# Optimization experiments

Hardware: AMD Instinct MI355X
Metric: run time of the kernel (lower is better)

## Reference

```python
import jax, jax.numpy as jnp
import numpy as np

INPUT_DIM = 1024; HID = 512; DSTATE = 64; EXPAND = 2; HDIM = 32; NHEAD = 8; DFF = 1024
DIN = EXPAND * HID          # 1024 inner dim
NH = DIN // HDIM            # 32 heads
G = 1; DCONV = 4            # ngroups, depthwise conv kernel
CONV_DIM = DIN + 2 * G * DSTATE          # 1152 (x, B, C go through conv)
DPROJ = 2 * DIN + 2 * G * DSTATE + NH    # 2208 (z, xBC, dt)
B = 2; L = 4096


def rmsnorm(x, w, eps=1e-5):
    return x * jax.lax.rsqrt(jnp.mean(x * x, axis=-1, keepdims=True) + eps) * w


def layernorm(x, w, b, eps=1e-5):
    m = jnp.mean(x, axis=-1, keepdims=True)
    v = jnp.mean((x - m) ** 2, axis=-1, keepdims=True)
    return (x - m) * jax.lax.rsqrt(v + eps) * w + b


def mamba_block(x, Wi, cw, cb, dtb, Alog, Dp, nw, Wo):
    # Mamba-2 style selective scan block (SISO, ngroups=1)
    Bb, Ln, _ = x.shape
    zxbcdt = x @ Wi                                   # [B,L,DPROJ]
    z = zxbcdt[..., :DIN]
    xBC = zxbcdt[..., DIN:DIN + CONV_DIM]
    dt = zxbcdt[..., DIN + CONV_DIM:]                 # [B,L,NH]
    # causal depthwise conv1d + silu
    xBC = jnp.transpose(xBC, (0, 2, 1))               # [B,C,L]
    xBC = jax.lax.conv_general_dilated(xBC, cw, (1,), [(DCONV - 1, 0)],
                                       feature_group_count=CONV_DIM) + cb[None, :, None]
    xBC = jax.nn.silu(jnp.transpose(xBC, (0, 2, 1)))
    xs = xBC[..., :DIN].reshape(Bb, Ln, NH, HDIM)     # [B,L,H,P]
    Bm = xBC[..., DIN:DIN + DSTATE]                   # [B,L,N]
    Cm = xBC[..., DIN + DSTATE:]                      # [B,L,N]
    dt = jax.nn.softplus(dt + dtb)                    # [B,L,H]
    decay = jnp.exp(dt * (-jnp.exp(Alog)))            # [B,L,H]
    dtx = dt[..., None] * xs                          # [B,L,H,P]

    def step(h, inp):
        dec, dx, Bt, Ct = inp                         # [B,H],[B,H,P],[B,N],[B,N]
        h = h * dec[:, :, None, None] + dx[..., None] * Bt[:, None, None, :]
        return h, jnp.einsum('bhpn,bn->bhp', h, Ct)

    h0 = jnp.zeros((Bb, NH, HDIM, DSTATE), x.dtype)
    _, ys = jax.lax.scan(step, h0, (jnp.moveaxis(decay, 1, 0), jnp.moveaxis(dtx, 1, 0),
                                    jnp.moveaxis(Bm, 1, 0), jnp.moveaxis(Cm, 1, 0)))
    y = jnp.moveaxis(ys, 0, 1) + Dp[None, None, :, None] * xs
    y = y.reshape(Bb, Ln, DIN)
    return rmsnorm(y * jax.nn.silu(z), nw) @ Wo       # gated RMSNorm + out proj


def transformer_layer(x, Wqkv, bqkv, Wo, bo, W1, b1, W2, b2, ln1w, ln1b, ln2w, ln2b):
    Bb, Ln, Dm = x.shape
    hd = Dm // NHEAD
    qkv = x @ Wqkv + bqkv
    q, k, v = jnp.split(qkv, 3, axis=-1)
    sp = lambda t: t.reshape(Bb, Ln, NHEAD, hd).transpose(0, 2, 1, 3)
    q, k, v = sp(q), sp(k), sp(v)
    att = jax.nn.softmax(jnp.einsum('bhqd,bhkd->bhqk', q, k) / np.float32(np.sqrt(hd)), axis=-1)
    o = jnp.einsum('bhqk,bhkd->bhqd', att, v).transpose(0, 2, 1, 3).reshape(Bb, Ln, Dm)
    x = layernorm(x + o @ Wo + bo, ln1w, ln1b)
    ff = jax.nn.gelu(x @ W1 + b1, approximate=False) @ W2 + b2
    return layernorm(x + ff, ln2w, ln2b)


def setup_inputs() -> dict:
    key = jax.random.key(0)
    ks = iter(jax.random.split(key, 64))
    w = lambda shape, s=0.02: jax.random.normal(next(ks), shape, jnp.float32) * s
    d = {}
    d['x'] = jax.random.normal(next(ks), (B, L, INPUT_DIM), jnp.float32)
    d['Wp'] = w((INPUT_DIM, HID)); d['bp'] = jnp.zeros((HID,), jnp.float32)
    for p in ('m1', 'm2'):
        d[p + '_Wi'] = w((HID, DPROJ))
        d[p + '_cw'] = w((CONV_DIM, 1, DCONV), 0.2)
        d[p + '_cb'] = jnp.zeros((CONV_DIM,), jnp.float32)
        d[p + '_dtb'] = jnp.log(jnp.expm1(jax.random.uniform(next(ks), (NH,), jnp.float32, 0.001, 0.1)))
        d[p + '_Alog'] = jnp.log(jax.random.uniform(next(ks), (NH,), jnp.float32, 1.0, 16.0))
        d[p + '_D'] = jnp.ones((NH,), jnp.float32)
        d[p + '_nw'] = jnp.ones((DIN,), jnp.float32)
        d[p + '_Wo'] = w((DIN, HID))
    d['n1_w'] = jnp.ones((HID,), jnp.float32); d['n2_w'] = jnp.ones((HID,), jnp.float32)
    d['ds_w'] = w((HID, HID, 3)); d['ds_b'] = jnp.zeros((HID,), jnp.float32)
    d['t_Wqkv'] = w((HID, 3 * HID)); d['t_bqkv'] = jnp.zeros((3 * HID,), jnp.float32)
    d['t_Wo'] = w((HID, HID)); d['t_bo'] = jnp.zeros((HID,), jnp.float32)
    d['t_W1'] = w((HID, DFF)); d['t_b1'] = jnp.zeros((DFF,), jnp.float32)
    d['t_W2'] = w((DFF, HID)); d['t_b2'] = jnp.zeros((HID,), jnp.float32)
    d['t_ln1w'] = jnp.ones((HID,), jnp.float32); d['t_ln1b'] = jnp.zeros((HID,), jnp.float32)
    d['t_ln2w'] = jnp.ones((HID,), jnp.float32); d['t_ln2b'] = jnp.zeros((HID,), jnp.float32)
    d['on_w'] = jnp.ones((HID,), jnp.float32); d['on_b'] = jnp.zeros((HID,), jnp.float32)
    return d


def reference(x, Wp, bp,
              m1_Wi, m1_cw, m1_cb, m1_dtb, m1_Alog, m1_D, m1_nw, m1_Wo,
              m2_Wi, m2_cw, m2_cb, m2_dtb, m2_Alog, m2_D, m2_nw, m2_Wo,
              n1_w, n2_w, ds_w, ds_b,
              t_Wqkv, t_bqkv, t_Wo, t_bo, t_W1, t_b1, t_W2, t_b2,
              t_ln1w, t_ln1b, t_ln2w, t_ln2b, on_w, on_b):
    x = x @ Wp + bp
    x = rmsnorm(mamba_block(x, m1_Wi, m1_cw, m1_cb, m1_dtb, m1_Alog, m1_D, m1_nw, m1_Wo) + x, n1_w)
    x = rmsnorm(mamba_block(x, m2_Wi, m2_cw, m2_cb, m2_dtb, m2_Alog, m2_D, m2_nw, m2_Wo) + x, n2_w)
    xt = jnp.transpose(x, (0, 2, 1))                  # [B,HID,L]
    xt = jax.lax.conv_general_dilated(xt, ds_w, (2,), [(1, 1)]) + ds_b[None, :, None]
    x = jnp.transpose(xt, (0, 2, 1))                  # [B,L/2,HID]
    x = transformer_layer(x, t_Wqkv, t_bqkv, t_Wo, t_bo, t_W1, t_b1, t_W2, t_b2,
                          t_ln1w, t_ln1b, t_ln2w, t_ln2b)
    return layernorm(x, on_w, on_b)
```

## Files before the change

### kernel.cpp

```cpp
#include <hip/hip_runtime.h>
#include <math.h>

#define DIN_   1024
#define DSTATE_ 64
#define NH_    32
#define HDIM_  32
#define CONVD_ 1152
#define DPROJ_ 2208
#define HID_   512
#define LSEQ_  4096
#define BB_    2
#define LT_    2048
#define NHEAD_ 8
#define HD_    64
#define DFF_   1024
#define LC_    256
#define NC_    16
#define NS_    4
#define KTS_   (LT_ / 64 / NS_)

typedef __attribute__((ext_vector_type(8))) short bf16x8;
typedef __attribute__((ext_vector_type(4))) short s16x4;
typedef __attribute__((ext_vector_type(4))) float f32x4;

__device__ __forceinline__ float siluf(float x) { return x / (1.f + __expf(-x)); }

__device__ __forceinline__ short f2b(float f) {
  union { float f; unsigned u; } v; v.f = f;
  unsigned r = (v.u + 0x7fffu + ((v.u >> 16) & 1u)) >> 16;
  return (short)r;
}

__device__ __forceinline__ short f2bt(float f) {
  union { float f; unsigned u; } v; v.f = f;
  return (short)(v.u >> 16);
}

__device__ __forceinline__ float b2f(short s) {
  union { unsigned u; float f; } v; v.u = ((unsigned)(unsigned short)s) << 16;
  return v.f;
}

__device__ __forceinline__ void gload16(const short* g, short* lds_base) {
#if __has_builtin(__builtin_amdgcn_global_load_lds)
  __builtin_amdgcn_global_load_lds((const __attribute__((address_space(1))) void*)g,
                                   (__attribute__((address_space(3))) void*)lds_base, 16, 0, 0);
#else
  int l = threadIdx.x & 63;
  ((bf16x8*)lds_base)[l] = *(const bf16x8*)g;
#endif
}

__device__ __forceinline__ void xcd_swz(int& bx, int& by, int& bz) {
  int nbx = gridDim.x, nby = gridDim.y;
  int nwg = nbx * nby * gridDim.z;
  int orig = (blockIdx.z * nby + blockIdx.y) * nbx + blockIdx.x;
  int q = nwg >> 3, r = nwg & 7;
  int xcd = orig & 7, lin = orig >> 3;
  int wg = (xcd < r ? xcd * (q + 1) : r * (q + 1) + (xcd - r) * q) + lin;
  bx = wg % nbx; wg /= nbx;
  by = wg % nby;
  bz = wg / nby;
}

__global__ void ec_f2b(const float* __restrict__ in, short* __restrict__ out, int n8)
{
  int i = blockIdx.x * 256 + threadIdx.x;
  if (i >= n8) return;
  const float4* p = (const float4*)(in + (size_t)i * 8);
  float4 a = p[0], b = p[1];
  bf16x8 o;
  o[0] = f2b(a.x); o[1] = f2b(a.y); o[2] = f2b(a.z); o[3] = f2b(a.w);
  o[4] = f2b(b.x); o[5] = f2b(b.y); o[6] = f2b(b.z); o[7] = f2b(b.w);
  *(bf16x8*)(out + (size_t)i * 8) = o;
}

__global__ __launch_bounds__(256) void ec_w2bt(const float* __restrict__ W,
                                               short* __restrict__ Wt, int K, int N)
{
  __shared__ float t[32][33];
  int k0 = blockIdx.x * 32, n0 = blockIdx.y * 32;
  int tx = threadIdx.x & 31, ty = threadIdx.x >> 5;
#pragma unroll
  for (int i = 0; i < 32; i += 8) t[ty + i][tx] = W[(size_t)(k0 + ty + i) * N + n0 + tx];
  __syncthreads();
#pragma unroll
  for (int i = 0; i < 32; i += 8) Wt[(size_t)(n0 + ty + i) * K + k0 + tx] = f2b(t[tx][ty + i]);
}

__global__ void ec_dswt(const float* __restrict__ w, short* __restrict__ wt)
{
  int idx = blockIdx.x * 256 + threadIdx.x;
  if (idx >= HID_ * 1536) return;
  int o = idx / 1536, r = idx % 1536;
  int k = r >> 9, i = r & 511;
  wt[idx] = f2b(w[((size_t)o * HID_ + i) * 3 + k]);
}

__global__ void ec_cwt(const float* __restrict__ cw, float* __restrict__ cwt)
{
  int idx = blockIdx.x * 256 + threadIdx.x;
  if (idx >= CONVD_ * 4) return;
  int j = idx / CONVD_, c = idx % CONVD_;
  cwt[idx] = cw[c * 4 + j];
}

__global__ __launch_bounds__(256) void ec_gemm16b(
    const short* __restrict__ A, const short* __restrict__ Wt,
    const float* __restrict__ bias, const float* __restrict__ res,
    float* __restrict__ Cf, short* __restrict__ Ch, short* __restrict__ Cv,
    int M, int N, int K, int act, int lda, long Az, int Mz)
{
  __shared__ short As_[2][4096];
  __shared__ short Bs_[2][4096];
  int bxi, byi, bzi;
  xcd_swz(bxi, byi, bzi);
  A += (size_t)bzi * Az;
  const int mz = bzi * Mz;
  const int tid = threadIdx.x;
  const int l = tid & 63, w = tid >> 6;
  const int m0 = byi * 64, n0 = bxi * 64;
  const int wm = (w >> 1) * 32, wn = (w & 1) * 32;
  const int lr = l & 15, lk = l >> 4;
  const int srow = w * 8 + (l >> 3);
  const int scol = ((l & 7) ^ (l >> 3)) * 8;
  const int rs0 = ((0 * 4 + lk) ^ (lr & 7)) * 8;
  const int rs1 = ((1 * 4 + lk) ^ (lr & 7)) * 8;

  f32x4 acc[2][2];
#pragma unroll
  for (int i = 0; i < 2; ++i)
#pragma unroll
    for (int j = 0; j < 2; ++j) acc[i][j] = f32x4{0.f, 0.f, 0.f, 0.f};

#pragma unroll
  for (int q = 0; q < 2; ++q) {
    int r = q * 32 + srow;
    const short* ga = A + (size_t)(m0 + r) * lda + scol;
    int rb = n0 + r; if (rb > N - 1) rb = N - 1;
    const short* gb = Wt + (size_t)rb * K + scol;
    gload16(ga, &As_[0][(q * 32 + w * 8) * 64]);
    gload16(gb, &Bs_[0][(q * 32 + w * 8) * 64]);
  }

  const int KT = K >> 6;
  for (int kt = 0; kt < KT; ++kt) {
    __syncthreads();
    if (kt + 1 < KT) {
      int k0 = (kt + 1) << 6;
      int nb = (kt + 1) & 1;
#pragma unroll
      for (int q = 0; q < 2; ++q) {
        int r = q * 32 + srow;
        const short* ga = A + (size_t)(m0 + r) * lda + k0 + scol;
        int rb = n0 + r; if (rb > N - 1) rb = N - 1;
        const short* gb = Wt + (size_t)rb * K + k0 + scol;
        gload16(ga, &As_[nb][(q * 32 + w * 8) * 64]);
        gload16(gb, &Bs_[nb][(q * 32 + w * 8) * 64]);
      }
    }
    int cb = kt & 1;
#pragma unroll
    for (int ksub = 0; ksub < 2; ++ksub) {
      const int rs = ksub ? rs1 : rs0;
      bf16x8 af[2], bfv[2];
#pragma unroll
      for (int mf = 0; mf < 2; ++mf)
        af[mf] = *(const bf16x8*)&As_[cb][(wm + mf * 16 + lr) * 64 + rs];
#pragma unroll
      for (int nf = 0; nf < 2; ++nf)
        bfv[nf] = *(const bf16x8*)&Bs_[cb][(wn + nf * 16 + lr) * 64 + rs];
#pragma unroll
      for (int mf = 0; mf < 2; ++mf)
#pragma unroll
        for (int nf = 0; nf < 2; ++nf)
          acc[mf][nf] = __builtin_amdgcn_mfma_f32_16x16x32_bf16(af[mf], bfv[nf], acc[mf][nf], 0, 0, 0);
    }
  }

  if (Cv && act == 2 && n0 >= 2 * HID_) {
    const int hh = (n0 - 2 * HID_) >> 6;
#pragma unroll
    for (int mf = 0; mf < 2; ++mf) {
      int mrow = m0 + wm + mf * 16 + lk * 4;
      int bb = mrow >> 11, tt = mrow & (LT_ - 1);
      size_t tb = (((size_t)(bb * NHEAD_ + hh) * (LT_ / 64) + (tt >> 6)) << 12) + (tt & 63);
#pragma unroll
      for (int nf = 0; nf < 2; ++nf) {
        int d = wn + nf * 16 + lr;
        float bv = bias ? bias[n0 + d] : 0.f;
        s16x4 ov;
#pragma unroll
        for (int r = 0; r < 4; ++r) ov[r] = f2b(acc[mf][nf][r] + bv);
        *(s16x4*)&Cv[tb + (size_t)d * 64] = ov;
      }
    }
    return;
  }

#pragma unroll
  for (int mf = 0; mf < 2; ++mf)
#pragma unroll
    for (int nf = 0; nf < 2; ++nf)
#pragma unroll
      for (int r = 0; r < 4; ++r) {
        int m = mz + m0 + wm + mf * 16 + lk * 4 + r;
        int n = n0 + wn + nf * 16 + lr;
        if (n < N) {
          float v = acc[mf][nf][r];
          if (bias) v += bias[n];
          if (act == 1) v = 0.5f * v * (1.f + erff(v * 0.70710678118f));
          else if (act == 2 && n < HID_) v *= 0.125f;
          if (res) v += res[(size_t)m * N + n];
          if (Cf) Cf[(size_t)m * N + n] = v;
          if (Ch) Ch[(size_t)m * N + n] = f2b(v);
        }
      }
}

static inline void gemm16b(hipStream_t s, const short* A, const short* Wt, const float* bias,
                           const float* res, float* Cf, short* Ch, int M, int N, int K, int act) {
  dim3 g((N + 63) / 64, M / 64), b(256);
  ec_gemm16b<<<g, b, 0, s>>>(A, Wt, bias, res, Cf, Ch, nullptr, M, N, K, act, K, 0, 0);
}

__global__ __launch_bounds__(512) void ec_dsfix(
    const short* __restrict__ x16, const short* __restrict__ wt,
    const float* __restrict__ bias, float* __restrict__ dsf, short* __restrict__ ds16)
{
  const int b = blockIdx.x, o = threadIdx.x;
  float v = bias[o];
#pragma unroll
  for (int k = 1; k < 3; ++k) {
    const short* xr = x16 + ((size_t)b * LSEQ_ + (k - 1)) * HID_;
    const short* wr = wt + (size_t)o * 1536 + k * 512;
    for (int i = 0; i < 512; i += 4) {
      s16x4 xv = *(const s16x4*)(xr + i);
      s16x4 wv = *(const s16x4*)(wr + i);
      v += b2f(xv[0]) * b2f(wv[0]) + b2f(xv[1]) * b2f(wv[1])
         + b2f(xv[2]) * b2f(wv[2]) + b2f(xv[3]) * b2f(wv[3]);
    }
  }
  dsf[(size_t)b * LT_ * HID_ + o] = v;
  ds16[(size_t)b * LT_ * HID_ + o] = f2b(v);
}

__global__ __launch_bounds__(256) void ec_conv1d_silu(
    const short* __restrict__ zx16, const float* __restrict__ cwt,
    const float* __restrict__ cb, short* __restrict__ xbc16,
    short* __restrict__ B16, short* __restrict__ C16)
{
  int idx = blockIdx.x * 256 + threadIdx.x;
  const int NG = CONVD_ / 4;
  if (idx >= BB_ * LSEQ_ * NG) return;
  int cg = idx % NG;
  int row = idx / NG;
  int l = row & (LSEQ_ - 1);
  int c0 = cg * 4;
  float4 cbv = *(const float4*)(cb + c0);
  float a0 = cbv.x, a1 = cbv.y, a2 = cbv.z, a3 = cbv.w;
#pragma unroll
  for (int j = 0; j < 4; ++j) {
    int ll = l - 3 + j;
    if (ll >= 0) {
      s16x4 xv = *(const s16x4*)(zx16 + (size_t)(row + ll - l) * DPROJ_ + DIN_ + c0);
      float4 wv = *(const float4*)(cwt + j * CONVD_ + c0);
      a0 += b2f(xv[0]) * wv.x;
      a1 += b2f(xv[1]) * wv.y;
      a2 += b2f(xv[2]) * wv.z;
      a3 += b2f(xv[3]) * wv.w;
    }
  }
  a0 = siluf(a0); a1 = siluf(a1); a2 = siluf(a2); a3 = siluf(a3);
  s16x4 pk; pk[0] = f2b(a0); pk[1] = f2b(a1); pk[2] = f2b(a2); pk[3] = f2b(a3);
  *(s16x4*)(xbc16 + (size_t)row * CONVD_ + c0) = pk;
  if (c0 >= DIN_) {
    int col = c0 - DIN_;
    if (col < 64) *(s16x4*)(B16 + (size_t)row * 64 + col) = pk;
    else          *(s16x4*)(C16 + (size_t)row * 64 + col - 64) = pk;
  }
}

__global__ __launch_bounds__(256) void ec_ssd_cumsum(
    const short* __restrict__ zx16, const float* __restrict__ dtb,
    const float* __restrict__ Alog, float* __restrict__ dts,
    float* __restrict__ lp, float* __restrict__ Pc)
{
  const int c = blockIdx.x, b = blockIdx.y, hg = blockIdx.z;
  const int t = threadIdx.x;
  const int lane = t & 63, wv = t >> 6;
  const size_t row = (size_t)b * LSEQ_ + (size_t)c * LC_ + t;
  const int h0 = hg * 8;
  __shared__ float wsum[4][8];

  bf16x8 dv = *(const bf16x8*)(zx16 + row * DPROJ_ + (DIN_ + CONVD_) + h0);
  float dt[8], cs[8];
#pragma unroll
  for (int j = 0; j < 8; ++j) {
    float x = b2f(dv[j]) + dtb[h0 + j];
    float sp = (x > 20.f) ? x : log1pf(__expf(x));
    dt[j] = sp;
    cs[j] = sp;
  }
#pragma unroll
  for (int d = 1; d < 64; d <<= 1) {
#pragma unroll
    for (int j = 0; j < 8; ++j) {
      float o = __shfl_up(cs[j], d, 64);
      if (lane >= d) cs[j] += o;
    }
  }
  if (lane == 63)
#pragma unroll
    for (int j = 0; j < 8; ++j) wsum[wv][j] = cs[j];
  __syncthreads();
#pragma unroll
  for (int j = 0; j < 8; ++j) {
    float base = 0.f;
#pragma unroll
    for (int k = 0; k < 3; ++k) if (k < wv) base += wsum[k][j];
    cs[j] += base;
  }
#pragma unroll
  for (int j = 0; j < 8; ++j) {
    int h = h0 + j;
    float lpv = -expf(Alog[h]) * cs[j];
    dts[row * NH_ + h] = dt[j];
    lp[row * NH_ + h] = lpv;
    if (t == LC_ - 1) Pc[(b * NC_ + c) * NH_ + h] = expf(lpv);
  }
}

__global__ __launch_bounds__(64) void ec_vt(
    const short* __restrict__ xbc16, const float* __restrict__ dts, short* __restrict__ VT)
{
  const int h = blockIdx.x, c = blockIdx.y, b = blockIdx.z;
  const int l = threadIdx.x;
  const size_t rowB = (size_t)b * LSEQ_ + (size_t)c * LC_;
  const size_t vtbase = (size_t)((b * NC_ + c) * NH_ + h) * 32;
  __shared__ float tile[32][33];
  for (int tt = 0; tt < 8; ++tt) {
#pragma unroll
    for (int i = 0; i < 16; ++i) {
      int r = i * 2 + (l >> 5);
      size_t row = rowB + tt * 32 + r;
      tile[r][l & 31] = b2f(xbc16[row * CONVD_ + h * 32 + (l & 31)]) * dts[row * NH_ + h];
    }
    __syncthreads();
#pragma unroll
    for (int j = 0; j < 16; ++j) {
      int p = j * 2 + (l >> 5);
      VT[(vtbase + p) * 256 + tt * 32 + (l & 31)] = f2b(tile[l & 31][p]);
    }
    __syncthreads();
  }
}

__device__ __forceinline__ float* state_ptr(float* stbuf, int b, int c, int h, int e)
{
  return stbuf + ((size_t)((b * NC_ + c) * NH_ + h)) * 2048 + e;
}

__global__ __launch_bounds__(64) void ec_ssd_p1(
    const short* __restrict__ B16, const short* __restrict__ VT,
    const float* __restrict__ lp, float* __restrict__ stbuf)
{
  const int h = blockIdx.x, c = blockIdx.y, b = blockIdx.z;
  const int l = threadIdx.x, lr = l & 15, lk = l >> 4;
  const size_t rowB = (size_t)b * LSEQ_ + (size_t)c * LC_;
  const size_t vtbase = (size_t)((b * NC_ + c) * NH_ + h) * 32;
  __shared__ short BT[64][264];
  for (int i = 0; i < 4; ++i) {
    int t = i * 64 + l;
#pragma unroll
    for (int g = 0; g < 8; ++g) {
      bf16x8 v = *(const bf16x8*)&B16[(rowB + t) * 64 + g * 8];
#pragma unroll
      for (int j = 0; j < 8; ++j) BT[g * 8 + j][t] = v[j];
    }
  }
  __syncthreads();
  const float lpE = lp[(rowB + LC_ - 1) * NH_ + h];
  f32x4 acc[2][4];
#pragma unroll
  for (int i = 0; i < 2; ++i)
#pragma unroll
    for (int j = 0; j < 4; ++j) acc[i][j] = f32x4{0.f, 0.f, 0.f, 0.f};

  for (int ks = 0; ks < 8; ++ks) {
    float wv[8];
#pragma unroll
    for (int j = 0; j < 8; ++j) {
      int t = ks * 32 + lk * 8 + j;
      wv[j] = __expf(lpE - lp[(rowB + t) * NH_ + h]);
    }
    bf16x8 af[2];
#pragma unroll
    for (int mf = 0; mf < 2; ++mf) {
      bf16x8 v = *(const bf16x8*)&VT[(vtbase + mf * 16 + lr) * 256 + ks * 32 + lk * 8];
#pragma unroll
      for (int j = 0; j < 8; ++j) af[mf][j] = f2b(b2f(v[j]) * wv[j]);
    }
#pragma unroll
    for (int nf = 0; nf < 4; ++nf) {
      bf16x8 bf = *(const bf16x8*)&BT[nf * 16 + lr][ks * 32 + lk * 8];
#pragma unroll
      for (int mf = 0; mf < 2; ++mf)
        acc[mf][nf] = __builtin_amdgcn_mfma_f32_16x16x32_bf16(af[mf], bf, acc[mf][nf], 0, 0, 0);
    }
  }
#pragma unroll
  for (int mf = 0; mf < 2; ++mf)
#pragma unroll
    for (int nf = 0; nf < 4; ++nf)
#pragma unroll
      for (int r = 0; r < 4; ++r) {
        int p = mf * 16 + lk * 4 + r, n = nf * 16 + lr;
        *state_ptr(stbuf, b, c, h, p * 64 + n) = acc[mf][nf][r];
      }
}

__global__ __launch_bounds__(512) void ec_scan_p2(
    float* __restrict__ stbuf, const float* __restrict__ Pc)
{
  const int h = blockIdx.x, b = blockIdx.y;
  const int tid = threadIdx.x;
  const int e = (tid >> 4) * 64 + (tid & 15) * 4;
  float h0 = 0.f, h1 = 0.f, h2 = 0.f, h3 = 0.f;
  for (int c = 0; c < NC_; ++c) {
    float* ptr = state_ptr(stbuf, b, c, h, e);
    float4 S = *(float4*)ptr;
    *(float4*)ptr = make_float4(h0, h1, h2, h3);
    float P = Pc[(b * NC_ + c) * NH_ + h];
    h0 = h0 * P + S.x;
    h1 = h1 * P + S.y;
    h2 = h2 * P + S.z;
    h3 = h3 * P + S.w;
  }
}

__global__ __launch_bounds__(256) void ec_ssd_p3(
    const short* __restrict__ B16, const short* __restrict__ C16,
    const short* __restrict__ VT, const float* __restrict__ lp,
    const short* __restrict__ xbc16, const float* __restrict__ Dp,
    float* __restrict__ stbuf, short* __restrict__ y16)
{
  const int h = blockIdx.x, c = blockIdx.y, b = blockIdx.z;
  const int tid = threadIdx.x;
  const int w = tid >> 6, l = tid & 63, lr = l & 15, lk = l >> 4;
  const size_t rowB = (size_t)b * LSEQ_ + (size_t)c * LC_;
  const size_t vtbase = (size_t)((b * NC_ + c) * NH_ + h) * 32;
  __shared__ short hI[32][72];
  __shared__ short Pl[4][64][72];

  for (int i = tid; i < 2048; i += 256)
    hI[i >> 6][i & 63] = f2b(*state_ptr(stbuf, b, c, h, i));
  __syncthreads();

  const int t0 = w * 64;
  bf16x8 cf[4][2];
#pragma unroll
  for (int tf = 0; tf < 4; ++tf)
#pragma unroll
    for (int ks = 0; ks < 2; ++ks)
      cf[tf][ks] = *(const bf16x8*)&C16[(rowB + t0 + tf * 16 + lr) * 64 + ks * 32 + lk * 8];

  f32x4 Y[4][2];
#pragma unroll
  for (int i = 0; i < 4; ++i)
#pragma unroll
    for (int j = 0; j < 2; ++j) Y[i][j] = f32x4{0.f, 0.f, 0.f, 0.f};
#pragma unroll
  for (int nf = 0; nf < 2; ++nf)
#pragma unroll
    for (int ks = 0; ks < 2; ++ks) {
      bf16x8 hf = *(const bf16x8*)&hI[nf * 16 + lr][ks * 32 + lk * 8];
#pragma unroll
      for (int mf = 0; mf < 4; ++mf)
        Y[mf][nf] = __builtin_amdgcn_mfma_f32_16x16x32_bf16(cf[mf][ks], hf, Y[mf][nf], 0, 0, 0);
    }
#pragma unroll
  for (int mf = 0; mf < 4; ++mf)
#pragma unroll
    for (int r = 0; r < 4; ++r) {
      float e = __expf(lp[(rowB + t0 + mf * 16 + lk * 4 + r) * NH_ + h]);
      Y[mf][0][r] *= e;
      Y[mf][1][r] *= e;
    }
  float tlp[4];
#pragma unroll
  for (int tf = 0; tf < 4; ++tf)
    tlp[tf] = lp[(rowB + t0 + tf * 16 + lr) * NH_ + h];

  for (int st = 0; st <= w; ++st) {
    const int s0 = st * 64;
#pragma unroll
    for (int half = 0; half < 2; ++half) {
      f32x4 ST[2][4];
#pragma unroll
      for (int i = 0; i < 2; ++i)
#pragma unroll
        for (int j = 0; j < 4; ++j) ST[i][j] = f32x4{0.f, 0.f, 0.f, 0.f};
#pragma unroll
      for (int sf2 = 0; sf2 < 2; ++sf2) {
        int sf = half * 2 + sf2;
#pragma unroll
        for (int ks = 0; ks < 2; ++ks) {
          bf16x8 bfr = *(const bf16x8*)&B16[(rowB + s0 + sf * 16 + lr) * 64 + ks * 32 + lk * 8];
#pragma unroll
          for (int tf = 0; tf < 4; ++tf)
            ST[sf2][tf] = __builtin_amdgcn_mfma_f32_16x16x32_bf16(bfr, cf[tf][ks], ST[sf2][tf], 0, 0, 0);
        }
      }
#pragma unroll
      for (int sf2 = 0; sf2 < 2; ++sf2) {
        int sf = half * 2 + sf2;
        float slp[4];
#pragma unroll
        for (int r = 0; r < 4; ++r)
          slp[r] = lp[(rowB + s0 + sf * 16 + lk * 4 + r) * NH_ + h];
#pragma unroll
        for (int tf = 0; tf < 4; ++tf) {
          float pv[4];
#pragma unroll
          for (int r = 0; r < 4; ++r) {
            pv[r] = ST[sf2][tf][r] * __expf(tlp[tf] - slp[r]);
            if (st == w && (sf * 16 + lk * 4 + r) > (tf * 16 + lr)) pv[r] = 0.f;
          }
          union { float f; unsigned u; } q0, q1, q2, q3;
          q0.f = pv[0]; q1.f = pv[1]; q2.f = pv[2]; q3.f = pv[3];
          uint2 pk;
          pk.x = (q0.u >> 16) | (q1.u & 0xffff0000u);
          pk.y = (q2.u >> 16) | (q3.u & 0xffff0000u);
          *(uint2*)&Pl[w][tf * 16 + lr][sf * 16 + lk * 4] = pk;
        }
      }
    }
    __builtin_amdgcn_sched_barrier(0);
    asm volatile("s_waitcnt lgkmcnt(0)" ::: "memory");
    __builtin_amdgcn_sched_barrier(0);
#pragma unroll
    for (int ks = 0; ks < 2; ++ks) {
      bf16x8 vf[2];
#pragma unroll
      for (int nf = 0; nf < 2; ++nf)
        vf[nf] = *(const bf16x8*)&VT[(vtbase + nf * 16 + lr) * 256 + s0 + ks * 32 + lk * 8];
#pragma unroll
      for (int mf = 0; mf < 4; ++mf) {
        bf16x8 pf = *(const bf16x8*)&Pl[w][mf * 16 + lr][ks * 32 + lk * 8];
#pragma unroll
        for (int nf = 0; nf < 2; ++nf)
          Y[mf][nf] = __builtin_amdgcn_mfma_f32_16x16x32_bf16(pf, vf[nf], Y[mf][nf], 0, 0, 0);
      }
    }
  }
  const float Dh = Dp[h];
#pragma unroll
  for (int mf = 0; mf < 4; ++mf)
#pragma unroll
    for (int r = 0; r < 4; ++r) {
      size_t yrow = rowB + t0 + mf * 16 + lk * 4 + r;
#pragma unroll
      for (int nf = 0; nf < 2; ++nf) {
        float xv = b2f(xbc16[yrow * CONVD_ + h * 32 + nf * 16 + lr]);
        y16[yrow * DIN_ + h * 32 + nf * 16 + lr] = f2b(Y[mf][nf][r] + Dh * xv);
      }
    }
}

__global__ __launch_bounds__(256) void ec_gate_rms16(
    const short* __restrict__ y16, const short* __restrict__ zx16,
    const float* __restrict__ nw, short* __restrict__ out)
{
  const int row = blockIdx.x;
  const int c0 = threadIdx.x * 4;
  s16x4 yv = *(const s16x4*)(y16 + (size_t)row * DIN_ + c0);
  s16x4 zv = *(const s16x4*)(zx16 + (size_t)row * DPROJ_ + c0);
  float v[4]; float ss = 0.f;
#pragma unroll
  for (int j = 0; j < 4; ++j) {
    float t = b2f(yv[j]) * siluf(b2f(zv[j]));
    v[j] = t; ss += t * t;
  }
#pragma unroll
  for (int m = 32; m >= 1; m >>= 1) ss += __shfl_xor(ss, m, 64);
  __shared__ float buf[4];
  if ((threadIdx.x & 63) == 0) buf[threadIdx.x >> 6] = ss;
  __syncthreads();
  ss = buf[0] + buf[1] + buf[2] + buf[3];
  float scale = rsqrtf(ss / (float)DIN_ + 1e-5f);
  float4 wv = *(const float4*)(nw + c0);
  s16x4 ov;
  ov[0] = f2b(v[0] * scale * wv.x);
  ov[1] = f2b(v[1] * scale * wv.y);
  ov[2] = f2b(v[2] * scale * wv.z);
  ov[3] = f2b(v[3] * scale * wv.w);
  *(s16x4*)(out + (size_t)row * DIN_ + c0) = ov;
}

__global__ __launch_bounds__(128) void ec_rmsadd16(
    const short* __restrict__ a16, const float* __restrict__ bres,
    const float* __restrict__ w, float* __restrict__ out, short* __restrict__ out16)
{
  const int row = blockIdx.x;
  const int c0 = threadIdx.x * 4;
  s16x4 av = *(const s16x4*)(a16 + (size_t)row * HID_ + c0);
  float4 brv = *(const float4*)(bres + (size_t)row * HID_ + c0);
  float v[4]; float ss = 0.f;
  v[0] = b2f(av[0]) + brv.x; v[1] = b2f(av[1]) + brv.y;
  v[2] = b2f(av[2]) + brv.z; v[3] = b2f(av[3]) + brv.w;
#pragma unroll
  for (int j = 0; j < 4; ++j) ss += v[j] * v[j];
#pragma unroll
  for (int m = 32; m >= 1; m >>= 1) ss += __shfl_xor(ss, m, 64);
  __shared__ float buf[2];
  if ((threadIdx.x & 63) == 0) buf[threadIdx.x >> 6] = ss;
  __syncthreads();
  ss = buf[0] + buf[1];
  float scale = rsqrtf(ss / (float)HID_ + 1e-5f);
  float4 wv = *(const float4*)(w + c0);
  float o0 = v[0] * scale * wv.x, o1 = v[1] * scale * wv.y;
  float o2 = v[2] * scale * wv.z, o3 = v[3] * scale * wv.w;
  *(float4*)(out + (size_t)row * HID_ + c0) = make_float4(o0, o1, o2, o3);
  s16x4 ov; ov[0] = f2b(o0); ov[1] = f2b(o1); ov[2] = f2b(o2); ov[3] = f2b(o3);
  *(s16x4*)(out16 + (size_t)row * HID_ + c0) = ov;
}

__global__ __launch_bounds__(128) void ec_ln16(
    const float* __restrict__ in, const float* __restrict__ w,
    const float* __restrict__ bb, float* __restrict__ out, short* __restrict__ out16)
{
  const int row = blockIdx.x;
  const float* ir = in + (size_t)row * HID_;
  float v[4]; float s = 0.f, s2 = 0.f;
#pragma unroll
  for (int j = 0; j < 4; ++j) {
    int c = j * 128 + threadIdx.x;
    float t = ir[c];
    v[j] = t; s += t; s2 += t * t;
  }
#pragma unroll
  for (int m = 32; m >= 1; m >>= 1) { s += __shfl_xor(s, m, 64); s2 += __shfl_xor(s2, m, 64); }
  __shared__ float buf[4];
  if ((threadIdx.x & 63) == 0) { int wi = threadIdx.x >> 6; buf[wi * 2] = s; buf[wi * 2 + 1] = s2; }
  __syncthreads();
  s = buf[0] + buf[2]; s2 = buf[1] + buf[3];
  float mean = s / (float)HID_;
  float var = s2 / (float)HID_ - mean * mean;
  float inv = rsqrtf(var + 1e-5f);
#pragma unroll
  for (int j = 0; j < 4; ++j) {
    int c = j * 128 + threadIdx.x;
    float o = (v[j] - mean) * inv * w[c] + bb[c];
    out[(size_t)row * HID_ + c] = o;
    if (out16) out16[(size_t)row * HID_ + c] = f2b(o);
  }
}

__global__ __launch_bounds__(512) void ec_attn16(
    const short* __restrict__ qkv, const short* __restrict__ vt16,
    short* __restrict__ Op, float2* __restrict__ ml)
{
  const int b = blockIdx.z & 1, split = blockIdx.z >> 1;
  const int h = blockIdx.y, qt = blockIdx.x;
  __shared__ short Kl[2][64 * 68];
  __shared__ short Vl[2][64 * 68];
  __shared__ short Pl[128 * 68];
  const int tid = threadIdx.x;
  const int l = tid & 63, w = tid >> 6;
  const int lr = l & 15, lk = l >> 4;

  const size_t qrow = (size_t)b * LT_ + qt * 128 + w * 16 + lr;
  bf16x8 qf[2];
  qf[0] = *(const bf16x8*)&qkv[qrow * 1536 + h * HD_ + lk * 8];
  qf[1] = *(const bf16x8*)&qkv[qrow * 1536 + h * HD_ + lk * 8 + 32];

  float mrun[4] = {-1e30f, -1e30f, -1e30f, -1e30f};
  float lsum[4] = {0.f, 0.f, 0.f, 0.f};
  f32x4 O[4];
#pragma unroll
  for (int df = 0; df < 4; ++df) O[df] = f32x4{0.f, 0.f, 0.f, 0.f};

  const int krow = tid >> 3, kcg = (tid & 7) * 8;
  const short* vtile = vt16 + (size_t)(b * NHEAD_ + h) * (LT_ / 64) * 4096;
  const int vofs = tid * 8;
  const int vlds = (tid >> 3) * 68 + (tid & 7) * 8;

  auto stageKV = [&](int kt, int bufi) {
    const size_t krbase = (size_t)b * LT_ + kt * 64;
    const short* kp = &qkv[(krbase + krow) * 1536 + HID_ + h * HD_ + kcg];
    *(bf16x8*)&Kl[bufi][krow * 68 + kcg] = *(const bf16x8*)kp;
    bf16x8 vv = *(const bf16x8*)&vtile[(size_t)kt * 4096 + vofs];
    *(bf16x8*)&Vl[bufi][vlds] = vv;
  };

  stageKV(split * KTS_, 0);
  __syncthreads();

  for (int i = 0; i < KTS_; ++i) {
    const int cur = i & 1;
    if (i + 1 < KTS_) stageKV(split * KTS_ + i + 1, cur ^ 1);

    f32x4 S[4];
#pragma unroll
    for (int nf = 0; nf < 4; ++nf) S[nf] = f32x4{0.f, 0.f, 0.f, 0.f};
#pragma unroll
    for (int ks = 0; ks < 2; ++ks)
#pragma unroll
      for (int nf = 0; nf < 4; ++nf) {
        bf16x8 kb = *(const bf16x8*)&Kl[cur][(nf * 16 + lr) * 68 + ks * 32 + lk * 8];
        S[nf] = __builtin_amdgcn_mfma_f32_16x16x32_bf16(qf[ks], kb, S[nf], 0, 0, 0);
      }

    int ok = 1;
#pragma unroll
    for (int nf = 0; nf < 4; ++nf)
#pragma unroll
      for (int r = 0; r < 4; ++r)
        ok &= (S[nf][r] <= mrun[r] + 8.f);
    if (!__all(ok)) {
      float fr[4];
#pragma unroll
      for (int r = 0; r < 4; ++r) {
        float mt = fmaxf(fmaxf(S[0][r], S[1][r]), fmaxf(S[2][r], S[3][r]));
        mt = fmaxf(mt, __shfl_xor(mt, 1));
        mt = fmaxf(mt, __shfl_xor(mt, 2));
        mt = fmaxf(mt, __shfl_xor(mt, 4));
        mt = fmaxf(mt, __shfl_xor(mt, 8));
        float mn = fmaxf(mrun[r], mt);
        fr[r] = __expf(mrun[r] - mn);
        mrun[r] = mn;
        lsum[r] *= fr[r];
      }
#pragma unroll
      for (int df = 0; df < 4; ++df) {
        O[df][0] *= fr[0]; O[df][1] *= fr[1]; O[df][2] *= fr[2]; O[df][3] *= fr[3];
      }
    }
#pragma unroll
    for (int nf = 0; nf < 4; ++nf)
#pragma unroll
      for (int r = 0; r < 4; ++r) {
        float p = __expf(S[nf][r] - mrun[r]);
        lsum[r] += p;
        Pl[(w * 16 + lk * 4 + r) * 68 + nf * 16 + lr] = f2bt(p);
      }

#pragma unroll
    for (int ks = 0; ks < 2; ++ks) {
      bf16x8 pa = *(const bf16x8*)&Pl[(w * 16 + lr) * 68 + ks * 32 + lk * 8];
#pragma unroll
      for (int df = 0; df < 4; ++df) {
        bf16x8 vb = *(const bf16x8*)&Vl[cur][(df * 16 + lr) * 68 + ks * 32 + lk * 8];
        O[df] = __builtin_amdgcn_mfma_f32_16x16x32_bf16(pa, vb, O[df], 0, 0, 0);
      }
    }
    __syncthreads();
  }

#pragma unroll
  for (int r = 0; r < 4; ++r) {
    lsum[r] += __shfl_xor(lsum[r], 1);
    lsum[r] += __shfl_xor(lsum[r], 2);
    lsum[r] += __shfl_xor(lsum[r], 4);
    lsum[r] += __shfl_xor(lsum[r], 8);
  }
  const size_t sstride = (size_t)BB_ * NHEAD_ * LT_;
  const size_t obase = (size_t)split * sstride + ((size_t)b * NHEAD_ + h) * LT_ + qt * 128 + w * 16;
#pragma unroll
  for (int df = 0; df < 4; ++df)
#pragma unroll
    for (int r = 0; r < 4; ++r)
      Op[(obase + lk * 4 + r) * 64 + df * 16 + lr] = f2b(O[df][r]);
  if (lr == 0)
#pragma unroll
    for (int r = 0; r < 4; ++r)
      ml[obase + lk * 4 + r] = make_float2(mrun[r], lsum[r]);
}

__global__ __launch_bounds__(256) void ec_attn_comb(
    const short* __restrict__ Op, const float2* __restrict__ ml, short* __restrict__ out)
{
  const int qt = blockIdx.x, h = blockIdx.y, b = blockIdx.z;
  const int r = threadIdx.x >> 2, c0 = (threadIdx.x & 3) * 16;
  const int qrow = qt * 64 + r;
  const size_t sstride = (size_t)BB_ * NHEAD_ * LT_;
  const size_t rb = ((size_t)b * NHEAD_ + h) * LT_ + qrow;
  float m[NS_], lv[NS_];
  float mmax = -1e30f;
#pragma unroll
  for (int s = 0; s < NS_; ++s) {
    float2 v = ml[rb + s * sstride];
    m[s] = v.x; lv[s] = v.y;
    mmax = fmaxf(mmax, m[s]);
  }
  float den = 0.f, wsc[NS_];
#pragma unroll
  for (int s = 0; s < NS_; ++s) { wsc[s] = __expf(m[s] - mmax); den += lv[s] * wsc[s]; }
  float inv = 1.f / den;
  float o[16];
#pragma unroll
  for (int i = 0; i < 16; ++i) o[i] = 0.f;
#pragma unroll
  for (int s = 0; s < NS_; ++s) {
    const short* p = Op + (rb + s * sstride) * 64 + c0;
    float wq = wsc[s];
#pragma unroll
    for (int i = 0; i < 4; ++i) {
      s16x4 v = *(const s16x4*)(p + i * 4);
      o[i * 4 + 0] += b2f(v[0]) * wq; o[i * 4 + 1] += b2f(v[1]) * wq;
      o[i * 4 + 2] += b2f(v[2]) * wq; o[i * 4 + 3] += b2f(v[3]) * wq;
    }
  }
  short* op = out + ((size_t)b * LT_ + qrow) * HID_ + h * HD_ + c0;
#pragma unroll
  for (int i = 0; i < 16; ++i) op[i] = f2b(o[i] * inv);
}

extern "C" void kernel_launch(void* const* d_in, const int* in_sizes, int n_in,
                              void* d_out, int out_size, void* d_ws, size_t ws_size,
                              hipStream_t stream)
{
  const float* x_in   = (const float*)d_in[0];
  const float* Wp     = (const float*)d_in[1];
  const float* bp     = (const float*)d_in[2];
  const float* m_Wi[2]   = {(const float*)d_in[3],  (const float*)d_in[11]};
  const float* m_cw[2]   = {(const float*)d_in[4],  (const float*)d_in[12]};
  const float* m_cb[2]   = {(const float*)d_in[5],  (const float*)d_in[13]};
  const float* m_dtb[2]  = {(const float*)d_in[6],  (const float*)d_in[14]};
  const float* m_Alog[2] = {(const float*)d_in[7],  (const float*)d_in[15]};
  const float* m_D[2]    = {(const float*)d_in[8],  (const float*)d_in[16]};
  const float* m_nw[2]   = {(const float*)d_in[9],  (const float*)d_in[17]};
  const float* m_Wo[2]   = {(const float*)d_in[10], (const float*)d_in[18]};
  const float* n_w[2]    = {(const float*)d_in[19], (const float*)d_in[20]};
  const float* ds_w   = (const float*)d_in[21];
  const float* ds_b   = (const float*)d_in[22];
  const float* t_Wqkv = (const float*)d_in[23];
  const float* t_bqkv = (const float*)d_in[24];
  const float* t_Wo   = (const float*)d_in[25];
  const float* t_bo   = (const float*)d_in[26];
  const float* t_W1   = (const float*)d_in[27];
  const float* t_b1   = (const float*)d_in[28];
  const float* t_W2   = (const float*)d_in[29];
  const float* t_b2   = (const float*)d_in[30];
  const float* t_ln1w = (const float*)d_in[31];
  const float* t_ln1b = (const float*)d_in[32];
  const float* t_ln2w = (const float*)d_in[33];
  const float* t_ln2b = (const float*)d_in[34];
  const float* on_w   = (const float*)d_in[35];
  const float* on_b   = (const float*)d_in[36];

  char* ws = (char*)d_ws;
  float* bx    = (float*)(ws + 0);
  short* zx16  = (short*)(ws + 16777216);
  float* stbuf = (float*)(ws + 16777216 + 36175872);
  short* xbc16 = (short*)(ws + 89128960);
  short* y16   = (short*)(ws + 126877696);
  short* VT    = (short*)(ws + 143654912);
  float* lp    = (float*)(ws + 160432128);
  float* dts   = (float*)(ws + 161480704);
  short* wslot = (short*)(ws + 162529280);
  float* Pc    = (float*)(ws + 165150720);
  float* cwt   = (float*)(ws + 165154816);

  short* B16 = wslot;
  short* C16 = wslot + 524288;
  short* a16buf = (short*)(ws + 126877696);

  short* x16     = (short*)(ws + 126877696);
  short* bx16    = (short*)(ws + 89128960);
  short* gated16 = (short*)(ws + 89128960 + 18874368);

  short*  Opart = (short*)(ws + 89128960);
  float2* mlbuf = (float2*)(ws + 89128960 + 33554432);

  char* tzone = ws + 16777216;
  short* ds16  = (short*)tzone;
  float* dsf   = (float*)(tzone + 4194304);
  short* qkv16 = (short*)(tzone + 12582912);
  short* att16 = (short*)(tzone + 25165824);
  float* bt1   = (float*)(tzone + 29360128);
  short* ln116 = (short*)(tzone + 37748736);
  float* bxt2  = (float*)(tzone + 41943040);
  short* ff16  = (short*)(tzone + 50331648);
  float* bt2   = (float*)(tzone + 58720256);
  short* vt16  = (short*)(tzone + 67108864);
  float* bxt3  = (float*)(ws + 89128960);

  const int MR = BB_ * LSEQ_;
  const int MT = BB_ * LT_;

  ec_f2b<<<(MR * 1024 / 8 + 255) / 256, 256, 0, stream>>>(x_in, x16, MR * 1024 / 8);
  ec_w2bt<<<dim3(1024 / 32, 512 / 32), 256, 0, stream>>>(Wp, wslot, 1024, 512);
  gemm16b(stream, x16, wslot, bp, nullptr, bx, bx16, MR, HID_, 1024, 0);

  for (int blk = 0; blk < 2; ++blk) {
    ec_w2bt<<<dim3(512 / 32, 2208 / 32), 256, 0, stream>>>(m_Wi[blk], wslot, 512, 2208);
    gemm16b(stream, bx16, wslot, nullptr, nullptr, nullptr, zx16, MR, DPROJ_, HID_, 0);
    ec_cwt<<<(CONVD_ * 4 + 255) / 256, 256, 0, stream>>>(m_cw[blk], cwt);
    ec_conv1d_silu<<<(MR * (CONVD_ / 4) + 255) / 256, 256, 0, stream>>>(
        zx16, cwt, m_cb[blk], xbc16, B16, C16);
    ec_ssd_cumsum<<<dim3(NC_, BB_, NH_ / 8), 256, 0, stream>>>(zx16, m_dtb[blk], m_Alog[blk], dts, lp, Pc);
    ec_vt<<<dim3(NH_, NC_, BB_), 64, 0, stream>>>(xbc16, dts, VT);
    ec_ssd_p1<<<dim3(NH_, NC_, BB_), 64, 0, stream>>>(B16, VT, lp, stbuf);
    ec_scan_p2<<<dim3(NH_, BB_), 512, 0, stream>>>(stbuf, Pc);
    ec_ssd_p3<<<dim3(NH_, NC_, BB_), 256, 0, stream>>>(B16, C16, VT, lp, xbc16, m_D[blk], stbuf, y16);
    ec_gate_rms16<<<MR, 256, 0, stream>>>(y16, zx16, m_nw[blk], gated16);
    ec_w2bt<<<dim3(1024 / 32, 512 / 32), 256, 0, stream>>>(m_Wo[blk], wslot, 1024, 512);
    gemm16b(stream, gated16, wslot, nullptr, nullptr, nullptr, a16buf, MR, HID_, DIN_, 0);
    ec_rmsadd16<<<MR, 128, 0, stream>>>(a16buf, bx, n_w[blk], bx, bx16);
  }

  ec_dswt<<<(HID_ * 1536 + 255) / 256, 256, 0, stream>>>(ds_w, wslot);
  {
    dim3 g(512 / 64, LT_ / 64, BB_), b(256);
    ec_gemm16b<<<g, b, 0, stream>>>(bx16 - 512, wslot, ds_b, nullptr, dsf, ds16, nullptr,
                                    LT_, HID_, 1536, 0, 1024, (long)LSEQ_ * HID_, LT_);
  }
  ec_dsfix<<<BB_, 512, 0, stream>>>(bx16, wslot, ds_b, dsf, ds16);

  ec_w2bt<<<dim3(512 / 32, 1536 / 32), 256, 0, stream>>>(t_Wqkv, wslot, 512, 1536);
  {
    dim3 g(1536 / 64, MT / 64), b(256);
    ec_gemm16b<<<g, b, 0, stream>>>(ds16, wslot, t_bqkv, nullptr, nullptr, qkv16, vt16,
                                    MT, 3 * HID_, HID_, 2, HID_, 0, 0);
  }
  ec_attn16<<<dim3(LT_ / 128, NHEAD_, BB_ * NS_), 512, 0, stream>>>(qkv16, vt16, Opart, mlbuf);
  ec_attn_comb<<<dim3(LT_ / 64, NHEAD_, BB_), 256, 0, stream>>>(Opart, mlbuf, att16);
  ec_w2bt<<<dim3(512 / 32, 512 / 32), 256, 0, stream>>>(t_Wo, wslot, 512, 512);
  gemm16b(stream, att16, wslot, t_bo, dsf, bt1, nullptr, MT, HID_, HID_, 0);
  ec_ln16<<<MT, 128, 0, stream>>>(bt1, t_ln1w, t_ln1b, bxt2, ln116);
  ec_w2bt<<<dim3(512 / 32, 1024 / 32), 256, 0, stream>>>(t_W1, wslot, 512, 1024);
  gemm16b(stream, ln116, wslot, t_b1, nullptr, nullptr, ff16, MT, DFF_, HID_, 1);
  ec_w2bt<<<dim3(1024 / 32, 512 / 32), 256, 0, stream>>>(t_W2, wslot, 1024, 512);
  gemm16b(stream, ff16, wslot, t_b2, bxt2, bt2, nullptr, MT, HID_, DFF_, 0);
  ec_ln16<<<MT, 128, 0, stream>>>(bt2, t_ln2w, t_ln2b, bxt3, nullptr);
  ec_ln16<<<MT, 128, 0, stream>>>(bxt3, on_w, on_b, (float*)d_out, nullptr);
}
```

Baseline: 573.6 us.

## Add 128x128-tile bf16 GEMM kernel for wide projection GEMMs

Adds a new MFMA GEMM kernel that uses 128x128 output tiles with a 32-wide K step and a 4x4 fragment accumulator per wave. It replaces the 64x64 GEMM for the Mamba in-projection, the QKV projection (including the transposed V write) and the FFN up-projection. Larger tiles raise arithmetic intensity and cut global and LDS traffic per flop. The cost is more register pressure and fewer blocks, which can hurt occupancy and tail balance. The V-transpose epilogue moves out of the old kernel into the new one.

```diff
diff --git a/kernel.cpp b/kernel.cpp
--- a/kernel.cpp
+++ b/kernel.cpp
@@ -108,7 +108,7 @@
 __global__ __launch_bounds__(256) void ec_gemm16b(
     const short* __restrict__ A, const short* __restrict__ Wt,
     const float* __restrict__ bias, const float* __restrict__ res,
-    float* __restrict__ Cf, short* __restrict__ Ch, short* __restrict__ Cv,
+    float* __restrict__ Cf, short* __restrict__ Ch,
     int M, int N, int K, int act, int lda, long Az, int Mz)
 {
   __shared__ short As_[2][4096];
@@ -178,26 +178,6 @@
     }
   }
 
-  if (Cv && act == 2 && n0 >= 2 * HID_) {
-    const int hh = (n0 - 2 * HID_) >> 6;
-#pragma unroll
-    for (int mf = 0; mf < 2; ++mf) {
-      int mrow = m0 + wm + mf * 16 + lk * 4;
-      int bb = mrow >> 11, tt = mrow & (LT_ - 1);
-      size_t tb = (((size_t)(bb * NHEAD_ + hh) * (LT_ / 64) + (tt >> 6)) << 12) + (tt & 63);
-#pragma unroll
-      for (int nf = 0; nf < 2; ++nf) {
-        int d = wn + nf * 16 + lr;
-        float bv = bias ? bias[n0 + d] : 0.f;
-        s16x4 ov;
-#pragma unroll
-        for (int r = 0; r < 4; ++r) ov[r] = f2b(acc[mf][nf][r] + bv);
-        *(s16x4*)&Cv[tb + (size_t)d * 64] = ov;
-      }
-    }
-    return;
-  }
-
 #pragma unroll
   for (int mf = 0; mf < 2; ++mf)
 #pragma unroll
@@ -221,7 +201,111 @@
 static inline void gemm16b(hipStream_t s, const short* A, const short* Wt, const float* bias,
                            const float* res, float* Cf, short* Ch, int M, int N, int K, int act) {
   dim3 g((N + 63) / 64, M / 64), b(256);
-  ec_gemm16b<<<g, b, 0, s>>>(A, Wt, bias, res, Cf, Ch, nullptr, M, N, K, act, K, 0, 0);
+  ec_gemm16b<<<g, b, 0, s>>>(A, Wt, bias, res, Cf, Ch, M, N, K, act, K, 0, 0);
+}
+
+__global__ __launch_bounds__(256) void ec_gemm128(
+    const short* __restrict__ A, const short* __restrict__ Wt,
+    const float* __restrict__ bias, short* __restrict__ Ch, short* __restrict__ Cv,
+    int M, int N, int K, int act)
+{
+  __shared__ short As_[2][4096];
+  __shared__ short Bs_[2][4096];
+  int bxi, byi, bzi;
+  xcd_swz(bxi, byi, bzi);
+  const int tid = threadIdx.x;
+  const int l = tid & 63, w = tid >> 6;
+  const int m0 = byi * 128, n0 = bxi * 128;
+  const int wm = (w >> 1) * 64, wn = (w & 1) * 64;
+  const int lr = l & 15, lk = l >> 4;
+  const int srow = w * 16 + (l >> 2);
+  const int rs = (lk ^ ((lr >> 1) & 3)) * 8;
+
+  f32x4 acc[4][4];
+#pragma unroll
+  for (int i = 0; i < 4; ++i)
+#pragma unroll
+    for (int j = 0; j < 4; ++j) acc[i][j] = f32x4{0.f, 0.f, 0.f, 0.f};
+
+#pragma unroll
+  for (int q = 0; q < 2; ++q) {
+    int grow = q * 64 + srow;
+    int gslot = ((l & 3) ^ ((grow >> 1) & 3)) * 8;
+    const short* ga = A + (size_t)(m0 + grow) * K + gslot;
+    int rb = n0 + grow; if (rb > N - 1) rb = N - 1;
+    const short* gb = Wt + (size_t)rb * K + gslot;
+    gload16(ga, &As_[0][(q * 64 + w * 16) * 32]);
+    gload16(gb, &Bs_[0][(q * 64 + w * 16) * 32]);
+  }
+
+  const int KT = K >> 5;
+  for (int kt = 0; kt < KT; ++kt) {
+    __syncthreads();
+    if (kt + 1 < KT) {
+      int k0 = (kt + 1) << 5;
+      int nb = (kt + 1) & 1;
+#pragma unroll
+      for (int q = 0; q < 2; ++q) {
+        int grow = q * 64 + srow;
+        int gslot = ((l & 3) ^ ((grow >> 1) & 3)) * 8;
+        const short* ga = A + (size_t)(m0 + grow) * K + k0 + gslot;
+        int rb = n0 + grow; if (rb > N - 1) rb = N - 1;
+        const short* gb = Wt + (size_t)rb * K + k0 + gslot;
+        gload16(ga, &As_[nb][(q * 64 + w * 16) * 32]);
+        gload16(gb, &Bs_[nb][(q * 64 + w * 16) * 32]);
+      }
+    }
+    int cb = kt & 1;
+    bf16x8 af[4], bfv[4];
+#pragma unroll
+    for (int f = 0; f < 4; ++f) {
+      af[f]  = *(const bf16x8*)&As_[cb][(wm + f * 16 + lr) * 32 + rs];
+      bfv[f] = *(const bf16x8*)&Bs_[cb][(wn + f * 16 + lr) * 32 + rs];
+    }
+#pragma unroll
+    for (int mf = 0; mf < 4; ++mf)
+#pragma unroll
+      for (int nf = 0; nf < 4; ++nf)
+        acc[mf][nf] = __builtin_amdgcn_mfma_f32_16x16x32_bf16(af[mf], bfv[nf], acc[mf][nf], 0, 0, 0);
+  }
+
+  if (Cv && act == 2 && n0 >= 2 * HID_) {
+#pragma unroll
+    for (int mf = 0; mf < 4; ++mf) {
+      int mrow = m0 + wm + mf * 16 + lk * 4;
+      int bb = mrow >> 11, tt = mrow & (LT_ - 1);
+#pragma unroll
+      for (int nf = 0; nf < 4; ++nf) {
+        int n = n0 + wn + nf * 16 + lr;
+        int vcol = n - 2 * HID_;
+        int hh = vcol >> 6, d = vcol & 63;
+        size_t tb = (((size_t)(bb * NHEAD_ + hh) * (LT_ / 64) + (tt >> 6)) << 12) + (tt & 63);
+        float bv = bias ? bias[n] : 0.f;
+        s16x4 ov;
+#pragma unroll
+        for (int r = 0; r < 4; ++r) ov[r] = f2b(acc[mf][nf][r] + bv);
+        *(s16x4*)&Cv[tb + (size_t)d * 64] = ov;
+      }
+    }
+    return;
+  }
+
+#pragma unroll
+  for (int mf = 0; mf < 4; ++mf)
+#pragma unroll
+    for (int nf = 0; nf < 4; ++nf)
+#pragma unroll
+      for (int r = 0; r < 4; ++r) {
+        int m = m0 + wm + mf * 16 + lk * 4 + r;
+        int n = n0 + wn + nf * 16 + lr;
+        if (n < N) {
+          float v = acc[mf][nf][r];
+          if (bias) v += bias[n];
+          if (act == 1) v = 0.5f * v * (1.f + erff(v * 0.70710678118f));
+          else if (act == 2 && n < HID_) v *= 0.125f;
+          Ch[(size_t)m * N + n] = f2b(v);
+        }
+      }
 }
 
 __global__ __launch_bounds__(512) void ec_dsfix(
@@ -896,7 +980,11 @@
 
   for (int blk = 0; blk < 2; ++blk) {
     ec_w2bt<<<dim3(512 / 32, 2208 / 32), 256, 0, stream>>>(m_Wi[blk], wslot, 512, 2208);
-    gemm16b(stream, bx16, wslot, nullptr, nullptr, nullptr, zx16, MR, DPROJ_, HID_, 0);
+    {
+      dim3 g((DPROJ_ + 127) / 128, MR / 128), b(256);
+      ec_gemm128<<<g, b, 0, stream>>>(bx16, wslot, nullptr, zx16, nullptr,
+                                      MR, DPROJ_, HID_, 0);
+    }
     ec_cwt<<<(CONVD_ * 4 + 255) / 256, 256, 0, stream>>>(m_cw[blk], cwt);
     ec_conv1d_silu<<<(MR * (CONVD_ / 4) + 255) / 256, 256, 0, stream>>>(
         zx16, cwt, m_cb[blk], xbc16, B16, C16);
@@ -914,16 +1002,16 @@
   ec_dswt<<<(HID_ * 1536 + 255) / 256, 256, 0, stream>>>(ds_w, wslot);
   {
     dim3 g(512 / 64, LT_ / 64, BB_), b(256);
-    ec_gemm16b<<<g, b, 0, stream>>>(bx16 - 512, wslot, ds_b, nullptr, dsf, ds16, nullptr,
+    ec_gemm16b<<<g, b, 0, stream>>>(bx16 - 512, wslot, ds_b, nullptr, dsf, ds16,
                                     LT_, HID_, 1536, 0, 1024, (long)LSEQ_ * HID_, LT_);
   }
   ec_dsfix<<<BB_, 512, 0, stream>>>(bx16, wslot, ds_b, dsf, ds16);
 
   ec_w2bt<<<dim3(512 / 32, 1536 / 32), 256, 0, stream>>>(t_Wqkv, wslot, 512, 1536);
   {
-    dim3 g(1536 / 64, MT / 64), b(256);
-    ec_gemm16b<<<g, b, 0, stream>>>(ds16, wslot, t_bqkv, nullptr, nullptr, qkv16, vt16,
-                                    MT, 3 * HID_, HID_, 2, HID_, 0, 0);
+    dim3 g(1536 / 128, MT / 128), b(256);
+    ec_gemm128<<<g, b, 0, stream>>>(ds16, wslot, t_bqkv, qkv16, vt16,
+                                    MT, 3 * HID_, HID_, 2);
   }
   ec_attn16<<<dim3(LT_ / 128, NHEAD_, BB_ * NS_), 512, 0, stream>>>(qkv16, vt16, Opart, mlbuf);
   ec_attn_comb<<<dim3(LT_ / 64, NHEAD_, BB_), 256, 0, stream>>>(Opart, mlbuf, att16);
@@ -931,7 +1019,11 @@
   gemm16b(stream, att16, wslot, t_bo, dsf, bt1, nullptr, MT, HID_, HID_, 0);
   ec_ln16<<<MT, 128, 0, stream>>>(bt1, t_ln1w, t_ln1b, bxt2, ln116);
   ec_w2bt<<<dim3(512 / 32, 1024 / 32), 256, 0, stream>>>(t_W1, wslot, 512, 1024);
-  gemm16b(stream, ln116, wslot, t_b1, nullptr, nullptr, ff16, MT, DFF_, HID_, 1);
+  {
+    dim3 g(DFF_ / 128, MT / 128), b(256);
+    ec_gemm128<<<g, b, 0, stream>>>(ln116, wslot, t_b1, ff16, nullptr,
+                                    MT, DFF_, HID_, 1);
+  }
   ec_w2bt<<<dim3(1024 / 32, 512 / 32), 256, 0, stream>>>(t_W2, wslot, 1024, 512);
   gemm16b(stream, ff16, wslot, t_b2, bxt2, bt2, nullptr, MT, HID_, DFF_, 0);
   ec_ln16<<<MT, 128, 0, stream>>>(bt2, t_ln2w, t_ln2b, bxt3, nullptr);
```

Measured after the change: 678.8 us. +18.3%, slower.
